# Optimization experiments

Measured on AMD Instinct MI355X. Metric: run time of the kernel, lower is better.

## Reference

```python
import jax, jax.numpy as jnp
import numpy as np

B, Q, T, H, W = 8, 100, 50, 256, 256
COST_MASK_W = 1.0  # init kwarg cost_mask
COST_DICE_W = 1.0  # init kwarg cost_dice


def setup_inputs() -> dict:
    key = jax.random.key(0)
    k1, k2 = jax.random.split(key)
    pred_masks = jax.random.normal(k1, (B, Q, H, W), dtype=jnp.float32)
    # binary GT masks (0/1), already at prediction resolution so nearest-interp is identity
    tgt_masks = jax.random.randint(k2, (B, T, H, W), 0, 2).astype(jnp.int32)
    return {"pred_masks": pred_masks, "tgt_masks": tgt_masks}


def reference(pred_masks, tgt_masks):
    # pred_masks: [B, Q, H, W] logits; tgt_masks: [B, T, H, W] binary
    b, q = pred_masks.shape[:2]
    x = pred_masks.reshape(b, q, -1)                      # [B, Q, HW]
    t = tgt_masks.reshape(b, tgt_masks.shape[1], -1).astype(x.dtype)  # [B, T, HW]
    hw = x.shape[-1]

    # batch_sigmoid_ce_loss: BCE-with-logits vs all-ones / all-zeros targets
    pos = jax.nn.softplus(-x)                             # BCE(x, 1)
    neg = jax.nn.softplus(x)                              # BCE(x, 0)
    cost_ce = (jnp.einsum('bqc,btc->bqt', pos, t)
               + jnp.einsum('bqc,btc->bqt', neg, 1.0 - t)) / hw

    # batch_dice_loss
    s = jax.nn.sigmoid(x)
    numerator = 2.0 * jnp.einsum('bqc,btc->bqt', s, t)
    denominator = s.sum(-1)[:, :, None] + t.sum(-1)[:, None, :]
    cost_dice = 1.0 - (numerator + 1.0) / (denominator + 1.0)

    # per-batch cost matrix C [B, Q, T]; the scipy Hungarian step is a
    # host-side CPU call outside the accelerator workload.
    return COST_MASK_W * cost_ce + COST_DICE_W * cost_dice
```

## Files before the change

kernel.cpp:

```cpp
#include <hip/hip_runtime.h>
#include <math.h>

#define B_ 8
#define Q_ 100
#define T_ 50
#define HW_ 65536
#define NSEG 128
#define SEG (HW_ / NSEG)
#define NK32 (SEG / 32)
#define NSTR 52

#define DSZ (B_ * Q_ * NSTR)
#define WS_D1 0
#define WS_D2 DSZ
#define WS_SNEG (2 * DSZ)
#define WS_ST (2 * DSZ + B_ * Q_)
#define WS_TOTAL (2 * DSZ + B_ * Q_ + B_ * T_)

typedef __attribute__((ext_vector_type(8))) short bf16x8;
typedef __attribute__((ext_vector_type(4))) float f32x4;

__device__ __forceinline__ unsigned short f2bf(float f) {
    union { float f; unsigned u; } v; v.f = f;
    unsigned r = v.u + 0x7FFF + ((v.u >> 16) & 1);
    return (unsigned short)(r >> 16);
}

__global__ void zero_ws(float* ws) {
    int i = blockIdx.x * blockDim.x + threadIdx.x;
    if (i < WS_TOTAL) ws[i] = 0.f;
}

__global__ __launch_bounds__(256, 2) void gemm_fused(const float* __restrict__ pred,
                                                     const int* __restrict__ tgt,
                                                     float* __restrict__ ws) {
    const int seg = blockIdx.x;
    const int b   = blockIdx.y;
    const int tid = threadIdx.x;
    const int wave = tid >> 6;
    const int lane = tid & 63;
    const int quad = lane >> 4;
    const int l16  = lane & 15;

    const float* xptr[2];
#pragma unroll
    for (int mt = 0; mt < 2; ++mt) {
        int m = (wave + mt * 4) * 16 + l16;
        int mr = m < Q_ ? m : Q_ - 1;
        xptr[mt] = pred + ((size_t)b * Q_ + mr) * HW_ + (size_t)seg * SEG + quad * 8;
    }
    const int* tptr[4];
    int ones[4];
#pragma unroll
    for (int nt = 0; nt < 4; ++nt) {
        int n = nt * 16 + l16;
        ones[nt] = (n == T_);
        int nr = n < T_ ? n : T_ - 1;
        tptr[nt] = tgt + ((size_t)b * T_ + nr) * HW_ + (size_t)seg * SEG + quad * 8;
    }

    f32x4 accx[2][4], accs[2][4];
#pragma unroll
    for (int mt = 0; mt < 2; ++mt)
#pragma unroll
        for (int nt = 0; nt < 4; ++nt) {
            accx[mt][nt] = (f32x4)(0.f);
            accs[mt][nt] = (f32x4)(0.f);
        }
    float sneg[2] = {0.f, 0.f};
    int stq[4] = {0, 0, 0, 0};

    float4 xrb[2][2][2];
    int4   trb[2][4][2];

    auto loadraw = [&](int ch, float4 xr[2][2], int4 tr[4][2]) {
        const int k = ch * 32;
#pragma unroll
        for (int nt = 0; nt < 4; ++nt) {
            tr[nt][0] = *(const int4*)(tptr[nt] + k);
            tr[nt][1] = *(const int4*)(tptr[nt] + k + 4);
        }
#pragma unroll
        for (int mt = 0; mt < 2; ++mt) {
            xr[mt][0] = *(const float4*)(xptr[mt] + k);
            xr[mt][1] = *(const float4*)(xptr[mt] + k + 4);
        }
    };

    auto compute = [&](float4 xr[2][2], int4 tr[4][2]) {
        bf16x8 xf[2], sf[2];
#pragma unroll
        for (int mt = 0; mt < 2; ++mt) {
            float sp = 0.f;
#pragma unroll
            for (int h = 0; h < 2; ++h)
#pragma unroll
                for (int e = 0; e < 4; ++e) {
                    float x = (&xr[mt][h].x)[e];
                    float ax = fabsf(x);
                    float ee = __expf(-ax);
                    float d = 1.f + ee;
                    float r1 = __builtin_amdgcn_rcpf(d);
                    float sg = (x >= 0.f) ? r1 : ee * r1;
                    sp += fmaxf(x, 0.f) + 0.69314718056f * __log2f(d);
                    xf[mt][h * 4 + e] = (short)f2bf(x);
                    sf[mt][h * 4 + e] = (short)f2bf(sg);
                }
            sneg[mt] += sp;
        }
        bf16x8 tf[4];
#pragma unroll
        for (int nt = 0; nt < 4; ++nt) {
            int cnt = 0;
#pragma unroll
            for (int h = 0; h < 2; ++h)
#pragma unroll
                for (int e = 0; e < 4; ++e) {
                    int v = (&tr[nt][h].x)[e];
                    tf[nt][h * 4 + e] = (v || ones[nt]) ? (short)0x3F80 : (short)0;
                    cnt += v;
                }
            stq[nt] += cnt;
        }
#pragma unroll
        for (int mt = 0; mt < 2; ++mt)
#pragma unroll
            for (int nt = 0; nt < 4; ++nt) {
                accx[mt][nt] = __builtin_amdgcn_mfma_f32_16x16x32_bf16(xf[mt], tf[nt], accx[mt][nt], 0, 0, 0);
                accs[mt][nt] = __builtin_amdgcn_mfma_f32_16x16x32_bf16(sf[mt], tf[nt], accs[mt][nt], 0, 0, 0);
            }
    };

    loadraw(0, xrb[0], trb[0]);
#pragma unroll 2
    for (int ch = 0; ch < NK32; ++ch) {
        const int cb = ch & 1;
        if (ch + 1 < NK32) loadraw(ch + 1, xrb[cb ^ 1], trb[cb ^ 1]);
        compute(xrb[cb], trb[cb]);
    }

#pragma unroll
    for (int mt = 0; mt < 2; ++mt) {
        float v = sneg[mt];
        v += __shfl_xor(v, 16);
        v += __shfl_xor(v, 32);
        int m = (wave + mt * 4) * 16 + l16;
        if (quad == 0 && m < Q_) atomicAdd(&ws[WS_SNEG + b * Q_ + m], v);
    }
    if (wave == 0) {
#pragma unroll
        for (int nt = 0; nt < 4; ++nt) {
            int vi = stq[nt];
            vi += __shfl_xor(vi, 16);
            vi += __shfl_xor(vi, 32);
            int n = nt * 16 + l16;
            if (quad == 0 && n < T_) atomicAdd(&ws[WS_ST + b * T_ + n], (float)vi);
        }
    }
#pragma unroll
    for (int mt = 0; mt < 2; ++mt) {
        int mtile = (wave + mt * 4) * 16;
#pragma unroll
        for (int nt = 0; nt < 4; ++nt) {
            int n = nt * 16 + l16;
#pragma unroll
            for (int r = 0; r < 4; ++r) {
                int m = mtile + quad * 4 + r;
                if (m < Q_) {
                    size_t idx = ((size_t)b * Q_ + m) * NSTR + n;
                    if (n < T_) atomicAdd(&ws[WS_D1 + idx], accx[mt][nt][r]);
                    if (n <= T_) atomicAdd(&ws[WS_D2 + idx], accs[mt][nt][r]);
                }
            }
        }
    }
}

__global__ void finalize(const float* __restrict__ ws, float* __restrict__ out) {
    int i = blockIdx.x * blockDim.x + threadIdx.x;
    if (i >= B_ * Q_ * T_) return;
    int b = i / (Q_ * T_);
    int r = i % (Q_ * T_);
    int q = r / T_;
    int t = r % T_;
    float dx   = ws[WS_D1 + ((size_t)b * Q_ + q) * NSTR + t];
    float ds   = ws[WS_D2 + ((size_t)b * Q_ + q) * NSTR + t];
    float ssum = ws[WS_D2 + ((size_t)b * Q_ + q) * NSTR + T_];
    float st   = ws[WS_ST + b * T_ + t];
    float sneg = ws[WS_SNEG + b * Q_ + q];
    float ce = (sneg - dx) * (1.f / (float)HW_);
    float dice = 1.f - (2.f * ds + 1.f) / (ssum + st + 1.f);
    out[i] = ce + dice;
}

extern "C" void kernel_launch(void* const* d_in, const int* in_sizes, int n_in,
                              void* d_out, int out_size, void* d_ws, size_t ws_size,
                              hipStream_t stream) {
    const float* pred = (const float*)d_in[0];
    const int* tgt = (const int*)d_in[1];
    float* ws = (float*)d_ws;
    float* out = (float*)d_out;

    zero_ws<<<(WS_TOTAL + 255) / 256, 256, 0, stream>>>(ws);
    dim3 g(NSEG, B_, 1);
    gemm_fused<<<g, 256, 0, stream>>>(pred, tgt, ws);
    finalize<<<(B_ * Q_ * T_ + 255) / 256, 256, 0, stream>>>(ws, out);
}
```

Before: 413.0 us.

## Bit-pack target masks in LDS and use 8-wave blocks with one M-tile per wave

Each block now reads its target segment once, packs it into bitmasks in shared memory with wave ballots, and counts target pixels with popcount. Previously every wave re-read the int32 targets from global memory for its MFMA operands. The block grows to 8 waves with a single 16-row M tile each, and the softplus sum is rebuilt algebraically from the x-sum (an extra MFMA ones-column) minus log2 of (1+exp(-x)). This cuts global target traffic and per-element transcendental work. In exchange it adds a barrier, LDS reads, and a softplus formula that can overflow in exp2 for very negative logits.

```diff
diff --git a/kernel.cpp b/kernel.cpp
--- a/kernel.cpp
+++ b/kernel.cpp
@@ -7,23 +7,30 @@
 #define HW_ 65536
 #define NSEG 128
 #define SEG (HW_ / NSEG)
-#define NK32 (SEG / 32)
+#define NCH (SEG / 32)
+#define NW 8
 #define NSTR 52
 
 #define DSZ (B_ * Q_ * NSTR)
 #define WS_D1 0
 #define WS_D2 DSZ
-#define WS_SNEG (2 * DSZ)
+#define WS_SLG (2 * DSZ)
 #define WS_ST (2 * DSZ + B_ * Q_)
 #define WS_TOTAL (2 * DSZ + B_ * Q_ + B_ * T_)
 
+#define LOG2E 1.44269504089f
+#define LN2 0.69314718056f
+
 typedef __attribute__((ext_vector_type(8))) short bf16x8;
 typedef __attribute__((ext_vector_type(4))) float f32x4;
+typedef __attribute__((ext_vector_type(4))) unsigned u32x4;
+union BFU { u32x4 u; bf16x8 h; };
 
-__device__ __forceinline__ unsigned short f2bf(float f) {
-    union { float f; unsigned u; } v; v.f = f;
-    unsigned r = v.u + 0x7FFF + ((v.u >> 16) & 1);
-    return (unsigned short)(r >> 16);
+__device__ __forceinline__ unsigned pack2bf(float a, float b) {
+    unsigned ua = __float_as_uint(a), ub = __float_as_uint(b);
+    ua = ua + 0x7fffu + ((ua >> 16) & 1u);
+    ub = ub + 0x7fffu + ((ub >> 16) & 1u);
+    return (ua >> 16) | (ub & 0xffff0000u);
 }
 
 __global__ void zero_ws(float* ws) {
@@ -31,7 +38,7 @@
     if (i < WS_TOTAL) ws[i] = 0.f;
 }
 
-__global__ __launch_bounds__(256, 2) void gemm_fused(const float* __restrict__ pred,
+__global__ __launch_bounds__(512, 3) void gemm_fused(const float* __restrict__ pred,
                                                      const int* __restrict__ tgt,
                                                      float* __restrict__ ws) {
     const int seg = blockIdx.x;
@@ -42,135 +49,114 @@
     const int quad = lane >> 4;
     const int l16  = lane & 15;
 
-    const float* xptr[2];
+    __shared__ unsigned tb[64][17];
+
+    const int m = wave * 16 + l16;
+    const int mr = m < Q_ ? m : Q_ - 1;
+    const float* xp = pred + ((size_t)b * Q_ + mr) * HW_ + (size_t)seg * SEG + quad * 8;
+
+    float4 x00 = *(const float4*)(xp);
+    float4 x01 = *(const float4*)(xp + 4);
+
+    const int* tbase = tgt + (size_t)b * T_ * HW_ + (size_t)seg * SEG;
+    for (int r = wave; r < T_; r += NW) {
+        float c = 0.f;
 #pragma unroll
-    for (int mt = 0; mt < 2; ++mt) {
-        int m = (wave + mt * 4) * 16 + l16;
-        int mr = m < Q_ ? m : Q_ - 1;
-        xptr[mt] = pred + ((size_t)b * Q_ + mr) * HW_ + (size_t)seg * SEG + quad * 8;
+        for (int wi = 0; wi < SEG / 64; ++wi) {
+            int v = tbase[(size_t)r * HW_ + wi * 64 + lane];
+            unsigned long long mask = __ballot(v != 0);
+            if (lane == 0) {
+                tb[r][wi * 2]     = (unsigned)mask;
+                tb[r][wi * 2 + 1] = (unsigned)(mask >> 32);
+                c += (float)__popcll(mask);
+            }
+        }
+        if (lane == 0) atomicAdd(&ws[WS_ST + b * T_ + r], c);
     }
-    const int* tptr[4];
-    int ones[4];
+    __syncthreads();
+
+    f32x4 accx[4], accs[4];
+#pragma unroll
+    for (int nt = 0; nt < 4; ++nt) { accx[nt] = (f32x4)(0.f); accs[nt] = (f32x4)(0.f); }
+    float slg = 0.f;
+
+    float4 xb[2][2];
+    unsigned twb[2][4];
+
+    auto load = [&](int ch, int pb) {
+        xb[pb][0] = *(const float4*)(xp + ch * 32);
+        xb[pb][1] = *(const float4*)(xp + ch * 32 + 4);
+#pragma unroll
+        for (int nt = 0; nt < 4; ++nt)
+            twb[pb][nt] = tb[nt * 16 + l16][ch];
+    };
+
+    auto compute = [&](int pb) {
+        BFU xf, sf;
+#pragma unroll
+        for (int h = 0; h < 2; ++h)
+#pragma unroll
+            for (int e = 0; e < 4; e += 2) {
+                float v0 = (&xb[pb][h].x)[e];
+                float v1 = (&xb[pb][h].x)[e + 1];
+                float e0 = __builtin_amdgcn_exp2f(-LOG2E * v0);
+                float e1 = __builtin_amdgcn_exp2f(-LOG2E * v1);
+                float d0 = 1.f + e0, d1 = 1.f + e1;
+                float s0 = __builtin_amdgcn_rcpf(d0);
+                float s1 = __builtin_amdgcn_rcpf(d1);
+                slg -= __builtin_amdgcn_logf(d0);
+                slg -= __builtin_amdgcn_logf(d1);
+                xf.u[h * 2 + e / 2] = pack2bf(v0, v1);
+                sf.u[h * 2 + e / 2] = pack2bf(s0, s1);
+            }
+        BFU tf[4];
+#pragma unroll
+        for (int nt = 0; nt < 4; ++nt) {
+            unsigned tw = twb[pb][nt];
+            if (nt == 3) tw = (l16 == 2) ? 0xffffffffu : tw;
+            unsigned byte = (tw >> (quad * 8)) & 0xffu;
+#pragma unroll
+            for (int j = 0; j < 4; ++j) {
+                unsigned b0 = (byte >> (2 * j)) & 1u;
+                unsigned b1 = (byte >> (2 * j + 1)) & 1u;
+                tf[nt].u[j] = b0 * 0x3F80u + b1 * 0x3F800000u;
+            }
+        }
+#pragma unroll
+        for (int nt = 0; nt < 4; ++nt) {
+            accx[nt] = __builtin_amdgcn_mfma_f32_16x16x32_bf16(xf.h, tf[nt].h, accx[nt], 0, 0, 0);
+            accs[nt] = __builtin_amdgcn_mfma_f32_16x16x32_bf16(sf.h, tf[nt].h, accs[nt], 0, 0, 0);
+        }
+    };
+
+    xb[0][0] = x00; xb[0][1] = x01;
+#pragma unroll
+    for (int nt = 0; nt < 4; ++nt) twb[0][nt] = tb[nt * 16 + l16][0];
+
+#pragma unroll 2
+    for (int ch = 0; ch < NCH; ++ch) {
+        const int pb = ch & 1;
+        if (ch + 1 < NCH) load(ch + 1, pb ^ 1);
+        compute(pb);
+    }
+
+    {
+        float v = slg;
+        v += __shfl_xor(v, 16);
+        v += __shfl_xor(v, 32);
+        if (quad == 0 && m < Q_) atomicAdd(&ws[WS_SLG + b * Q_ + m], v);
+    }
 #pragma unroll
     for (int nt = 0; nt < 4; ++nt) {
         int n = nt * 16 + l16;
-        ones[nt] = (n == T_);
-        int nr = n < T_ ? n : T_ - 1;
-        tptr[nt] = tgt + ((size_t)b * T_ + nr) * HW_ + (size_t)seg * SEG + quad * 8;
-    }
-
-    f32x4 accx[2][4], accs[2][4];
+        if (n > T_) continue;
 #pragma unroll
-    for (int mt = 0; mt < 2; ++mt)
-#pragma unroll
-        for (int nt = 0; nt < 4; ++nt) {
-            accx[mt][nt] = (f32x4)(0.f);
-            accs[mt][nt] = (f32x4)(0.f);
-        }
-    float sneg[2] = {0.f, 0.f};
-    int stq[4] = {0, 0, 0, 0};
-
-    float4 xrb[2][2][2];
-    int4   trb[2][4][2];
-
-    auto loadraw = [&](int ch, float4 xr[2][2], int4 tr[4][2]) {
-        const int k = ch * 32;
-#pragma unroll
-        for (int nt = 0; nt < 4; ++nt) {
-            tr[nt][0] = *(const int4*)(tptr[nt] + k);
-            tr[nt][1] = *(const int4*)(tptr[nt] + k + 4);
-        }
-#pragma unroll
-        for (int mt = 0; mt < 2; ++mt) {
-            xr[mt][0] = *(const float4*)(xptr[mt] + k);
-            xr[mt][1] = *(const float4*)(xptr[mt] + k + 4);
-        }
-    };
-
-    auto compute = [&](float4 xr[2][2], int4 tr[4][2]) {
-        bf16x8 xf[2], sf[2];
-#pragma unroll
-        for (int mt = 0; mt < 2; ++mt) {
-            float sp = 0.f;
-#pragma unroll
-            for (int h = 0; h < 2; ++h)
-#pragma unroll
-                for (int e = 0; e < 4; ++e) {
-                    float x = (&xr[mt][h].x)[e];
-                    float ax = fabsf(x);
-                    float ee = __expf(-ax);
-                    float d = 1.f + ee;
-                    float r1 = __builtin_amdgcn_rcpf(d);
-                    float sg = (x >= 0.f) ? r1 : ee * r1;
-                    sp += fmaxf(x, 0.f) + 0.69314718056f * __log2f(d);
-                    xf[mt][h * 4 + e] = (short)f2bf(x);
-                    sf[mt][h * 4 + e] = (short)f2bf(sg);
-                }
-            sneg[mt] += sp;
-        }
-        bf16x8 tf[4];
-#pragma unroll
-        for (int nt = 0; nt < 4; ++nt) {
-            int cnt = 0;
-#pragma unroll
-            for (int h = 0; h < 2; ++h)
-#pragma unroll
-                for (int e = 0; e < 4; ++e) {
-                    int v = (&tr[nt][h].x)[e];
-                    tf[nt][h * 4 + e] = (v || ones[nt]) ? (short)0x3F80 : (short)0;
-                    cnt += v;
-                }
-            stq[nt] += cnt;
-        }
-#pragma unroll
-        for (int mt = 0; mt < 2; ++mt)
-#pragma unroll
-            for (int nt = 0; nt < 4; ++nt) {
-                accx[mt][nt] = __builtin_amdgcn_mfma_f32_16x16x32_bf16(xf[mt], tf[nt], accx[mt][nt], 0, 0, 0);
-                accs[mt][nt] = __builtin_amdgcn_mfma_f32_16x16x32_bf16(sf[mt], tf[nt], accs[mt][nt], 0, 0, 0);
-            }
-    };
-
-    loadraw(0, xrb[0], trb[0]);
-#pragma unroll 2
-    for (int ch = 0; ch < NK32; ++ch) {
-        const int cb = ch & 1;
-        if (ch + 1 < NK32) loadraw(ch + 1, xrb[cb ^ 1], trb[cb ^ 1]);
-        compute(xrb[cb], trb[cb]);
-    }
-
-#pragma unroll
-    for (int mt = 0; mt < 2; ++mt) {
-        float v = sneg[mt];
-        v += __shfl_xor(v, 16);
-        v += __shfl_xor(v, 32);
-        int m = (wave + mt * 4) * 16 + l16;
-        if (quad == 0 && m < Q_) atomicAdd(&ws[WS_SNEG + b * Q_ + m], v);
-    }
-    if (wave == 0) {
-#pragma unroll
-        for (int nt = 0; nt < 4; ++nt) {
-            int vi = stq[nt];
-            vi += __shfl_xor(vi, 16);
-            vi += __shfl_xor(vi, 32);
-            int n = nt * 16 + l16;
-            if (quad == 0 && n < T_) atomicAdd(&ws[WS_ST + b * T_ + n], (float)vi);
-        }
-    }
-#pragma unroll
-    for (int mt = 0; mt < 2; ++mt) {
-        int mtile = (wave + mt * 4) * 16;
-#pragma unroll
-        for (int nt = 0; nt < 4; ++nt) {
-            int n = nt * 16 + l16;
-#pragma unroll
-            for (int r = 0; r < 4; ++r) {
-                int m = mtile + quad * 4 + r;
-                if (m < Q_) {
-                    size_t idx = ((size_t)b * Q_ + m) * NSTR + n;
-                    if (n < T_) atomicAdd(&ws[WS_D1 + idx], accx[mt][nt][r]);
-                    if (n <= T_) atomicAdd(&ws[WS_D2 + idx], accs[mt][nt][r]);
-                }
+        for (int r = 0; r < 4; ++r) {
+            int mm = wave * 16 + quad * 4 + r;
+            if (mm < Q_) {
+                size_t idx = ((size_t)b * Q_ + mm) * NSTR + n;
+                atomicAdd(&ws[WS_D1 + idx], accx[nt][r]);
+                atomicAdd(&ws[WS_D2 + idx], accs[nt][r]);
             }
         }
     }
@@ -185,9 +171,11 @@
     int t = r % T_;
     float dx   = ws[WS_D1 + ((size_t)b * Q_ + q) * NSTR + t];
     float ds   = ws[WS_D2 + ((size_t)b * Q_ + q) * NSTR + t];
+    float sumx = ws[WS_D1 + ((size_t)b * Q_ + q) * NSTR + T_];
     float ssum = ws[WS_D2 + ((size_t)b * Q_ + q) * NSTR + T_];
+    float slg  = ws[WS_SLG + b * Q_ + q];
     float st   = ws[WS_ST + b * T_ + t];
-    float sneg = ws[WS_SNEG + b * Q_ + q];
+    float sneg = sumx - LN2 * slg;
     float ce = (sneg - dx) * (1.f / (float)HW_);
     float dice = 1.f - (2.f * ds + 1.f) / (ssum + st + 1.f);
     out[i] = ce + dice;
@@ -203,6 +191,6 @@
 
     zero_ws<<<(WS_TOTAL + 255) / 256, 256, 0, stream>>>(ws);
     dim3 g(NSEG, B_, 1);
-    gemm_fused<<<g, 256, 0, stream>>>(pred, tgt, ws);
+    gemm_fused<<<g, 512, 0, stream>>>(pred, tgt, ws);
     finalize<<<(B_ * Q_ * T_ + 255) / 256, 256, 0, stream>>>(ws, out);
 }
```

Result: slower. 452.4 us (+9.5%).
